# Performance work log

Measured on AMD Instinct MI355X. Metric: run time of the kernel, lower is better.

## Reference

```python
import jax, jax.numpy as jnp
import numpy as np

S, B, D, H = 2048, 2, 1024, 16
DK = D // H  # 64

def setup_inputs() -> dict:
    key0 = jax.random.key(0)
    ks = jax.random.split(key0, 11)
    scale = 0.02
    inp = {
        'query': jax.random.normal(ks[0], (S, B, D), jnp.float32),
        'key':   jax.random.normal(ks[1], (S, B, D), jnp.float32),
        'value': jax.random.normal(ks[2], (S, B, D), jnp.float32),
        # nn.Linear weights stored torch-style [out_features, in_features]
        'Wq': jax.random.normal(ks[3], (H * DK, D), jnp.float32) * scale,
        'bq': jnp.zeros((H * DK,), jnp.float32),
        'Wk': jax.random.normal(ks[4], (H * DK, D), jnp.float32) * scale,
        'bk': jnp.zeros((H * DK,), jnp.float32),
        'Wv': jax.random.normal(ks[5], (H * DK, D), jnp.float32) * scale,
        'bv': jnp.zeros((H * DK,), jnp.float32),
        'Wo': jax.random.normal(ks[6], (D, D), jnp.float32) * scale,
        'bo': jnp.zeros((D,), jnp.float32),
    }
    return inp

def _proj(x, W, b):
    # x: [S,B,D] -> [S,B,H,DK]
    y = jnp.einsum('sbd,ed->sbe', x, W) + b
    return y.reshape(x.shape[0], x.shape[1], H, DK)

def reference(query, key, value, Wq, bq, Wk, bk, Wv, bv, Wo, bo):
    q = _proj(query, Wq, bq)   # [S,B,H,DK]
    k = _proj(key,   Wk, bk)
    v = _proj(value, Wv, bv)
    # NOTE: original forward never applies self.scale -> unscaled QK^T (faithful)
    scores = jnp.einsum('ibhd,jbhd->ijbh', q, k)      # [Sq,Sk,B,H]
    attn = jax.nn.softmax(scores, axis=1)             # softmax over key axis j
    x = jnp.einsum('ijbh,jbhd->ibhd', attn, v)        # [S,B,H,DK]
    x = x.reshape(q.shape[0], q.shape[1], H * DK)     # [S,B,D]
    out = jnp.einsum('sbd,ed->sbe', x, Wo) + bo       # [S,B,D]
    return out
```

## Files before the change

kernel.cpp:

```cpp
#include <hip/hip_runtime.h>
#include <stdint.h>

#define S_LEN  2048
#define BATCH  2
#define DMODEL 1024
#define NHEAD  16
#define DKH    64

typedef __attribute__((ext_vector_type(8))) __bf16 bf16x8;
typedef __attribute__((ext_vector_type(4))) float  f32x4;
typedef unsigned short u16;
typedef unsigned int   u32;

#if __has_builtin(__builtin_amdgcn_exp2f)
#define EXP2(x) __builtin_amdgcn_exp2f(x)
#else
#define EXP2(x) __expf(0.69314718055994531f * (x))
#endif

#define SWAP32(a, b) asm("v_permlane32_swap_b32 %0, %1" : "+v"(a), "+v"(b))
#define SWAP16(a, b) asm("v_permlane16_swap_b32 %0, %1" : "+v"(a), "+v"(b))

__device__ __forceinline__ u16 f2bf(float f) {
  union { float f; u32 u; } v; v.f = f;
  u32 r = v.u + 0x7fffu + ((v.u >> 16) & 1u);
  return (u16)(r >> 16);
}

__global__ void cvt_all(const float4* __restrict__ q, const float4* __restrict__ k,
                        const float4* __restrict__ v,
                        const float4* __restrict__ wq, const float4* __restrict__ wk,
                        const float4* __restrict__ wv, const float4* __restrict__ wo,
                        ushort4* __restrict__ dst) {
  const int NX4 = (S_LEN * BATCH * DMODEL) / 4;
  const int NW4 = (DMODEL * DMODEL) / 4;
  int i = blockIdx.x * blockDim.x + threadIdx.x;
  const float4* src;
  int off;
  if (i < 3 * NX4) {
    src = (i < NX4) ? q : (i < 2 * NX4) ? k : v;
    off = i & (NX4 - 1);
  } else {
    int j = i - 3 * NX4;
    int t = j >> 18;
    src = (t == 0) ? wq : (t == 1) ? wk : (t == 2) ? wv : wo;
    off = j & (NW4 - 1);
  }
  float4 val = src[off];
  ushort4 o;
  o.x = f2bf(val.x); o.y = f2bf(val.y); o.z = f2bf(val.z); o.w = f2bf(val.w);
  dst[i] = o;
}

__global__ __launch_bounds__(256, 2)
void gemm_qkv(const u16* __restrict__ Abase, const u16* __restrict__ Wbase,
              const float* __restrict__ b0, const float* __restrict__ b1,
              const float* __restrict__ b2, u16* __restrict__ Obase) {
  __shared__ __align__(16) u16 As[128 * 32];
  __shared__ __align__(16) u16 Bs[128 * 32];

  const int L = blockIdx.x + (blockIdx.y << 3) + (blockIdx.z << 8);
  const int xcd = L & 7, sl = L >> 3;
  const int z  = sl >> 5;
  const int y  = xcd * 4 + ((sl >> 3) & 3);
  const int nx = sl & 7;

  const u16* A = Abase + (size_t)z * (S_LEN * BATCH * DMODEL);
  const u16* W = Wbase + (size_t)z * (DMODEL * DMODEL);
  const float* bias = (z == 0) ? b0 : (z == 1) ? b1 : b2;
  u16* O = Obase + (size_t)z * (S_LEN * BATCH * DMODEL);
  const float scl = (z == 0) ? 1.4426950408889634f : 1.0f;

  const int tid  = threadIdx.x;
  const int wave = tid >> 6, lane = tid & 63;
  const int quad = lane >> 4, lcol = lane & 15;
  const int m0 = y * 128, n0 = nx * 128;
  const int wm = (wave >> 1) * 64, wn = (wave & 1) * 64;

  f32x4 acc[4][4] = {};

  for (int k0 = 0; k0 < DMODEL; k0 += 32) {
#pragma unroll
    for (int r = 0; r < 2; ++r) {
      int idx = r * 256 + tid;
      int row = idx >> 2, col = (idx & 3) * 8;
      const u16* gA = A + (size_t)(m0 + row) * DMODEL + k0 + col;
      const u16* gW = W + (size_t)(n0 + row) * DMODEL + k0 + col;
      u16* lA = As + (size_t)(r * 256 + (tid & 192)) * 8;
      u16* lB = Bs + (size_t)(r * 256 + (tid & 192)) * 8;
      __builtin_amdgcn_global_load_lds((const __attribute__((address_space(1))) void*)gA,
                                       (__attribute__((address_space(3))) void*)lA, 16, 0, 0);
      __builtin_amdgcn_global_load_lds((const __attribute__((address_space(1))) void*)gW,
                                       (__attribute__((address_space(3))) void*)lB, 16, 0, 0);
    }
    __syncthreads();

    const u16* aBase = As + (wm + lcol) * 32 + quad * 8;
    const u16* bBase = Bs + (wn + lcol) * 32 + quad * 8;
    bf16x8 af[4], bfr[4];
#pragma unroll
    for (int i = 0; i < 4; ++i) af[i]  = *(const bf16x8*)(aBase + i * 16 * 32);
#pragma unroll
    for (int j = 0; j < 4; ++j) bfr[j] = *(const bf16x8*)(bBase + j * 16 * 32);
#pragma unroll
    for (int i = 0; i < 4; ++i)
#pragma unroll
      for (int j = 0; j < 4; ++j)
        acc[i][j] = __builtin_amdgcn_mfma_f32_16x16x32_bf16(af[i], bfr[j], acc[i][j], 0, 0, 0);
    __syncthreads();
  }

#pragma unroll
  for (int i = 0; i < 4; ++i) {
#pragma unroll
    for (int j = 0; j < 4; ++j) {
      int n = n0 + wn + j * 16 + lcol;
      int h = n >> 6, dk = n & 63;
      float bv = bias[n];
#pragma unroll
      for (int r = 0; r < 4; ++r) {
        int m = m0 + wm + i * 16 + quad * 4 + r;
        int s = m >> 1, b = m & 1;
        O[((size_t)(b * NHEAD + h) * S_LEN + s) * DKH + dk] = f2bf((acc[i][j][r] + bv) * scl);
      }
    }
  }
}

__global__ __launch_bounds__(256, 2)
void gemm_o(const u16* __restrict__ A, const u16* __restrict__ W,
            const float* __restrict__ bias, float* __restrict__ O) {
  __shared__ __align__(16) u16 As[128 * 32];
  __shared__ __align__(16) u16 Bs[64 * 32];

  const int L = blockIdx.x + (blockIdx.y << 4);
  const int xcd = L & 7, sl = L >> 3;
  const int y = xcd * 4 + (sl >> 4);
  const int x = sl & 15;

  const int tid  = threadIdx.x;
  const int wave = tid >> 6, lane = tid & 63;
  const int quad = lane >> 4, lcol = lane & 15;
  const int m0 = y * 128, n0 = x * 64;
  const int wm = (wave >> 1) * 64, wn = (wave & 1) * 32;

  f32x4 acc[4][2] = {};

  for (int k0 = 0; k0 < DMODEL; k0 += 32) {
#pragma unroll
    for (int r = 0; r < 2; ++r) {
      int idx = r * 256 + tid;
      int row = idx >> 2, col = (idx & 3) * 8;
      const u16* gA = A + (size_t)(m0 + row) * DMODEL + k0 + col;
      u16* lA = As + (size_t)(r * 256 + (tid & 192)) * 8;
      __builtin_amdgcn_global_load_lds((const __attribute__((address_space(1))) void*)gA,
                                       (__attribute__((address_space(3))) void*)lA, 16, 0, 0);
    }
    {
      int row = tid >> 2, col = (tid & 3) * 8;
      const u16* gW = W + (size_t)(n0 + row) * DMODEL + k0 + col;
      u16* lB = Bs + (size_t)(tid & 192) * 8;
      __builtin_amdgcn_global_load_lds((const __attribute__((address_space(1))) void*)gW,
                                       (__attribute__((address_space(3))) void*)lB, 16, 0, 0);
    }
    __syncthreads();

    const u16* aBase = As + (wm + lcol) * 32 + quad * 8;
    const u16* bBase = Bs + (wn + lcol) * 32 + quad * 8;
    bf16x8 af[4], bfr[2];
#pragma unroll
    for (int i = 0; i < 4; ++i) af[i]  = *(const bf16x8*)(aBase + i * 16 * 32);
#pragma unroll
    for (int j = 0; j < 2; ++j) bfr[j] = *(const bf16x8*)(bBase + j * 16 * 32);
#pragma unroll
    for (int i = 0; i < 4; ++i)
#pragma unroll
      for (int j = 0; j < 2; ++j)
        acc[i][j] = __builtin_amdgcn_mfma_f32_16x16x32_bf16(af[i], bfr[j], acc[i][j], 0, 0, 0);
    __syncthreads();
  }

#pragma unroll
  for (int i = 0; i < 4; ++i) {
#pragma unroll
    for (int j = 0; j < 2; ++j) {
      int n = n0 + wn + j * 16 + lcol;
      float bv = bias[n];
#pragma unroll
      for (int r = 0; r < 4; ++r) {
        int m = m0 + wm + i * 16 + quad * 4 + r;
        O[(size_t)m * DMODEL + n] = acc[i][j][r] + bv;
      }
    }
  }
}

__global__ __launch_bounds__(512, 2)
void attn_kernel(const u16* __restrict__ Q, const u16* __restrict__ K,
                 const u16* __restrict__ V, u16* __restrict__ O) {
  __shared__ __align__(16) u16 smem[9216 + 9216];
  __shared__ float ls2[4][4][16];
  u16* Ks  = smem;
  u16* Vts = smem + 9216;

  const int tid  = threadIdx.x;
  const int wave = tid >> 6, lane = tid & 63;
  const int quad = lane >> 4, lcol = lane & 15;
  const int qg = wave & 3;
  const int kh = wave >> 2;

  const int L = blockIdx.x + (blockIdx.y << 3);
  const int xcd = L & 7, slot = L >> 3;
  const int bh = xcd * 4 + (slot >> 3);
  const int q0 = (slot & 7) * 256;

  const size_t headOff = (size_t)bh * S_LEN * DKH;
  const u16* Qg = Q + headOff;
  const u16* Kg = K + headOff;
  const u16* Vg = V + headOff;

  bf16x8 qf[4][2];
#pragma unroll
  for (int s = 0; s < 4; ++s)
#pragma unroll
    for (int kc = 0; kc < 2; ++kc)
      qf[s][kc] = *(const bf16x8*)(Qg + (size_t)(q0 + qg * 64 + s * 16 + lcol) * DKH +
                                   kc * 32 + quad * 8);

  const int krow  = tid >> 3, kch = tid & 7;
  const int vhalf = lane >> 5, vkp = lane & 31;
  const int vo    = wave;

  uint4 kr0 = *(const uint4*)(Kg + (size_t)krow * DKH + kch * 8);
  uint4 kr1 = *(const uint4*)(Kg + (size_t)(S_LEN / 2 + krow) * DKH + kch * 8);
  uint4 vr0, vr1;
  {
    const u16* vp = Vg + (size_t)(vhalf * (S_LEN / 2) + 2 * vkp) * DKH + 8 * vo;
    vr0 = *(const uint4*)vp;
    vr1 = *(const uint4*)(vp + DKH);
  }

  f32x4 o_acc[4][4] = {};
  float lsum[4] = {0.f, 0.f, 0.f, 0.f};

  for (int it = 0; it < 16; ++it) {
    *(uint4*)(Ks + (size_t)krow * 72 + kch * 8)        = kr0;
    *(uint4*)(Ks + (size_t)(64 + krow) * 72 + kch * 8) = kr1;
    {
      u16* vd = Vts + vhalf * 4608;
#pragma unroll
      for (int jj = 0; jj < 4; ++jj) {
        u32 aw = ((const u32*)&vr0)[jj], bw = ((const u32*)&vr1)[jj];
        *(u32*)(vd + (size_t)(8 * vo + 2 * jj) * 72 + 2 * vkp)     = __builtin_amdgcn_perm(bw, aw, 0x05040100u);
        *(u32*)(vd + (size_t)(8 * vo + 2 * jj + 1) * 72 + 2 * vkp) = __builtin_amdgcn_perm(bw, aw, 0x07060302u);
      }
    }
    __syncthreads();

    if (it < 15) {
      int nb = (it + 1) * 64;
      kr0 = *(const uint4*)(Kg + (size_t)(nb + krow) * DKH + kch * 8);
      kr1 = *(const uint4*)(Kg + (size_t)(S_LEN / 2 + nb + krow) * DKH + kch * 8);
      const u16* vp = Vg + (size_t)(vhalf * (S_LEN / 2) + nb + 2 * vkp) * DKH + 8 * vo;
      vr0 = *(const uint4*)vp;
      vr1 = *(const uint4*)(vp + DKH);
    }

    const u16* kb = Ks  + kh * 64 * 72;
    const u16* vb = Vts + kh * 4608;

#pragma unroll
    for (int g = 0; g < 2; ++g) {
      bf16x8 ak[2][2];
#pragma unroll
      for (int jb = 0; jb < 2; ++jb)
#pragma unroll
        for (int kc = 0; kc < 2; ++kc)
          ak[jb][kc] = *(const bf16x8*)(kb + (g * 32 + jb * 16 + lcol) * 72 + kc * 32 + quad * 8);
      f32x4 sc[2][4] = {};
      __builtin_amdgcn_s_setprio(1);
#pragma unroll
      for (int kc = 0; kc < 2; ++kc)
#pragma unroll
        for (int jb = 0; jb < 2; ++jb)
#pragma unroll
          for (int s = 0; s < 4; ++s)
            sc[jb][s] = __builtin_amdgcn_mfma_f32_16x16x32_bf16(ak[jb][kc], qf[s][kc], sc[jb][s], 0, 0, 0);
      __builtin_amdgcn_s_setprio(0);

      bf16x8 pa[4];
#pragma unroll
      for (int s = 0; s < 4; ++s) {
        u32 ww[2][2];
#pragma unroll
        for (int jb = 0; jb < 2; ++jb) {
          float p0 = EXP2(sc[jb][s][0]);
          float p1 = EXP2(sc[jb][s][1]);
          float p2 = EXP2(sc[jb][s][2]);
          float p3 = EXP2(sc[jb][s][3]);
          lsum[s] += (p0 + p1) + (p2 + p3);
          asm("v_cvt_pk_bf16_f32 %0, %1, %2" : "=v"(ww[jb][0]) : "v"(p0), "v"(p1));
          asm("v_cvt_pk_bf16_f32 %0, %1, %2" : "=v"(ww[jb][1]) : "v"(p2), "v"(p3));
        }
        u32 a0 = ww[0][0], b0 = ww[1][0];
        SWAP32(a0, b0); SWAP16(a0, b0);
        u32 a1 = ww[0][1], b1 = ww[1][1];
        SWAP32(a1, b1); SWAP16(a1, b1);
        union { u32 u[4]; bf16x8 v; } f;
        f.u[0] = a0; f.u[1] = a1; f.u[2] = b0; f.u[3] = b1;
        pa[s] = f.v;
      }

      bf16x8 bv[4];
#pragma unroll
      for (int jd = 0; jd < 4; ++jd)
        bv[jd] = *(const bf16x8*)(vb + (jd * 16 + lcol) * 72 + g * 32 + quad * 8);
      __builtin_amdgcn_s_setprio(1);
#pragma unroll
      for (int s = 0; s < 4; ++s)
#pragma unroll
        for (int jd = 0; jd < 4; ++jd)
          o_acc[s][jd] = __builtin_amdgcn_mfma_f32_16x16x32_bf16(pa[s], bv[jd], o_acc[s][jd], 0, 0, 0);
      __builtin_amdgcn_s_setprio(0);
    }

    __syncthreads();
  }

#pragma unroll
  for (int s = 0; s < 4; ++s) {
    lsum[s] += __shfl_xor(lsum[s], 16);
    lsum[s] += __shfl_xor(lsum[s], 32);
  }

  float* scr = (float*)smem;
  const int cbase = (qg * 64 + lane) * 32;
  if (kh == 1) {
#pragma unroll
    for (int s = 0; s < 2; ++s)
#pragma unroll
      for (int jd = 0; jd < 4; ++jd)
        *(f32x4*)(scr + cbase + (s * 4 + jd) * 4) = o_acc[s][jd];
    if (lane < 16) {
#pragma unroll
      for (int s = 0; s < 4; ++s) ls2[qg][s][lane] = lsum[s];
    }
  }
  __syncthreads();
  if (kh == 0) {
#pragma unroll
    for (int s = 0; s < 2; ++s)
#pragma unroll
      for (int jd = 0; jd < 4; ++jd)
        o_acc[s][jd] += *(const f32x4*)(scr + cbase + (s * 4 + jd) * 4);
  }
  __syncthreads();
  if (kh == 1) {
#pragma unroll
    for (int s = 2; s < 4; ++s)
#pragma unroll
      for (int jd = 0; jd < 4; ++jd)
        *(f32x4*)(scr + cbase + ((s - 2) * 4 + jd) * 4) = o_acc[s][jd];
  }
  __syncthreads();
  if (kh == 0) {
#pragma unroll
    for (int s = 2; s < 4; ++s)
#pragma unroll
      for (int jd = 0; jd < 4; ++jd)
        o_acc[s][jd] += *(const f32x4*)(scr + cbase + ((s - 2) * 4 + jd) * 4);

    float tot[4];
#pragma unroll
    for (int s = 0; s < 4; ++s) tot[s] = lsum[s] + ls2[qg][s][lcol];

    const int b = bh >> 4, hh = bh & 15;
#pragma unroll
    for (int s = 0; s < 4; ++s) {
#pragma unroll
      for (int r = 0; r < 4; ++r) {
        float inv = 1.f / __shfl(tot[s], quad * 4 + r);
        int sq = q0 + qg * 64 + s * 16 + quad * 4 + r;
#pragma unroll
        for (int jd = 0; jd < 4; ++jd) {
          int dk = jd * 16 + lcol;
          O[((size_t)(sq * BATCH + b)) * DMODEL + hh * DKH + dk] = f2bf(o_acc[s][jd][r] * inv);
        }
      }
    }
  }
}

extern "C" void kernel_launch(void* const* d_in, const int* in_sizes, int n_in,
                              void* d_out, int out_size, void* d_ws, size_t ws_size,
                              hipStream_t stream) {
  const float* q  = (const float*)d_in[0];
  const float* k  = (const float*)d_in[1];
  const float* v  = (const float*)d_in[2];
  const float* Wq = (const float*)d_in[3];
  const float* bq = (const float*)d_in[4];
  const float* Wk = (const float*)d_in[5];
  const float* bk = (const float*)d_in[6];
  const float* Wv = (const float*)d_in[7];
  const float* bv = (const float*)d_in[8];
  const float* Wo = (const float*)d_in[9];
  const float* bo = (const float*)d_in[10];

  const int NX = S_LEN * BATCH * DMODEL;
  const int NW = DMODEL * DMODEL;

  u16* ws  = (u16*)d_ws;
  u16* Xq  = ws;
  u16* Wqb = Xq  + 3 * (size_t)NX;
  u16* Qb  = Wqb + 4 * (size_t)NW;
  u16* Xo  = Qb  + 3 * (size_t)NX;

  u16* Wob = Wqb + 3 * (size_t)NW;
  u16* Kb  = Qb + NX, *Vb = Qb + 2 * (size_t)NX;

  const int n4 = (3 * NX + 4 * NW) / 4;
  cvt_all<<<n4 / 256, 256, 0, stream>>>((const float4*)q, (const float4*)k, (const float4*)v,
                                        (const float4*)Wq, (const float4*)Wk, (const float4*)Wv,
                                        (const float4*)Wo, (ushort4*)ws);

  dim3 gqkv(DMODEL / 128, (S_LEN * BATCH) / 128, 3);
  gemm_qkv<<<gqkv, 256, 0, stream>>>(Xq, Wqb, bq, bk, bv, Qb);

  dim3 ga(S_LEN / 256, BATCH * NHEAD);
  attn_kernel<<<ga, 512, 0, stream>>>(Qb, Kb, Vb, Xo);

  dim3 go(DMODEL / 64, (S_LEN * BATCH) / 128);
  gemm_o<<<go, 256, 0, stream>>>(Xo, Wob, bo, (float*)d_out);
}
```

Before: 214.3 us.

## Double-buffer attention K/V in LDS with direct global-to-LDS K loads

Each attention block now covers 128 queries instead of 256, so the grid doubles and launch bounds target more resident blocks. K tiles are loaded straight into LDS with global_load_lds using an XOR swizzle instead of padding, and K and V use double-buffered LDS so one barrier per iteration suffices. The V transpose write is moved after compute to overlap with it, and the final reduction drops to a single exchange round. This adds more K/V reloads per head and LDS pressure, and relies on the swizzle and buffer indexing being correct.

```diff
diff --git a/kernel.cpp b/kernel.cpp
--- a/kernel.cpp
+++ b/kernel.cpp
@@ -195,13 +195,12 @@
   }
 }
 
-__global__ __launch_bounds__(512, 2)
+__global__ __launch_bounds__(512, 4)
 void attn_kernel(const u16* __restrict__ Q, const u16* __restrict__ K,
                  const u16* __restrict__ V, u16* __restrict__ O) {
-  __shared__ __align__(16) u16 smem[9216 + 9216];
-  __shared__ float ls2[4][4][16];
-  u16* Ks  = smem;
-  u16* Vts = smem + 9216;
+  __shared__ __align__(16) u16 Ks[2][128 * 64];
+  __shared__ __align__(16) u16 Vts[2][2 * 4608];
+  __shared__ float ls2[4][2][16];
 
   const int tid  = threadIdx.x;
   const int wave = tid >> 6, lane = tid & 63;
@@ -209,65 +208,72 @@
   const int qg = wave & 3;
   const int kh = wave >> 2;
 
-  const int L = blockIdx.x + (blockIdx.y << 3);
+  const int L = blockIdx.x + (blockIdx.y << 4);
   const int xcd = L & 7, slot = L >> 3;
-  const int bh = xcd * 4 + (slot >> 3);
-  const int q0 = (slot & 7) * 256;
+  const int bh = xcd * 4 + (slot >> 4);
+  const int q0 = (slot & 15) * 128;
 
   const size_t headOff = (size_t)bh * S_LEN * DKH;
   const u16* Qg = Q + headOff;
   const u16* Kg = K + headOff;
   const u16* Vg = V + headOff;
 
-  bf16x8 qf[4][2];
-#pragma unroll
-  for (int s = 0; s < 4; ++s)
+  bf16x8 qf[2][2];
+#pragma unroll
+  for (int s = 0; s < 2; ++s)
 #pragma unroll
     for (int kc = 0; kc < 2; ++kc)
-      qf[s][kc] = *(const bf16x8*)(Qg + (size_t)(q0 + qg * 64 + s * 16 + lcol) * DKH +
+      qf[s][kc] = *(const bf16x8*)(Qg + (size_t)(q0 + qg * 32 + s * 16 + lcol) * DKH +
                                    kc * 32 + quad * 8);
 
-  const int krow  = tid >> 3, kch = tid & 7;
-  const int vhalf = lane >> 5, vkp = lane & 31;
-  const int vo    = wave;
-
-  uint4 kr0 = *(const uint4*)(Kg + (size_t)krow * DKH + kch * 8);
-  uint4 kr1 = *(const uint4*)(Kg + (size_t)(S_LEN / 2 + krow) * DKH + kch * 8);
-  uint4 vr0, vr1;
+  const int krow = tid >> 3;
+  const int kcs  = (((tid & 7) ^ ((tid >> 3) & 7))) * 8;
+  const int kdst = (tid & 448) * 8;
+  const int vhalf = lane >> 5, vkp = lane & 31, vo = wave;
+
   {
     const u16* vp = Vg + (size_t)(vhalf * (S_LEN / 2) + 2 * vkp) * DKH + 8 * vo;
-    vr0 = *(const uint4*)vp;
-    vr1 = *(const uint4*)(vp + DKH);
-  }
-
-  f32x4 o_acc[4][4] = {};
-  float lsum[4] = {0.f, 0.f, 0.f, 0.f};
+    uint4 vr0 = *(const uint4*)vp;
+    uint4 vr1 = *(const uint4*)(vp + DKH);
+    __builtin_amdgcn_global_load_lds(
+        (const __attribute__((address_space(1))) void*)(Kg + (size_t)krow * DKH + kcs),
+        (__attribute__((address_space(3))) void*)(Ks[0] + kdst), 16, 0, 0);
+    __builtin_amdgcn_global_load_lds(
+        (const __attribute__((address_space(1))) void*)(Kg + (size_t)(S_LEN / 2 + krow) * DKH + kcs),
+        (__attribute__((address_space(3))) void*)(Ks[0] + 4096 + kdst), 16, 0, 0);
+    u16* vd = Vts[0] + vhalf * 4608;
+#pragma unroll
+    for (int jj = 0; jj < 4; ++jj) {
+      u32 aw = ((const u32*)&vr0)[jj], bw = ((const u32*)&vr1)[jj];
+      *(u32*)(vd + (size_t)(8 * vo + 2 * jj) * 72 + 2 * vkp)     = __builtin_amdgcn_perm(bw, aw, 0x05040100u);
+      *(u32*)(vd + (size_t)(8 * vo + 2 * jj + 1) * 72 + 2 * vkp) = __builtin_amdgcn_perm(bw, aw, 0x07060302u);
+    }
+  }
+
+  f32x4 o_acc[2][4] = {};
+  float lsum[2] = {0.f, 0.f};
 
   for (int it = 0; it < 16; ++it) {
-    *(uint4*)(Ks + (size_t)krow * 72 + kch * 8)        = kr0;
-    *(uint4*)(Ks + (size_t)(64 + krow) * 72 + kch * 8) = kr1;
-    {
-      u16* vd = Vts + vhalf * 4608;
-#pragma unroll
-      for (int jj = 0; jj < 4; ++jj) {
-        u32 aw = ((const u32*)&vr0)[jj], bw = ((const u32*)&vr1)[jj];
-        *(u32*)(vd + (size_t)(8 * vo + 2 * jj) * 72 + 2 * vkp)     = __builtin_amdgcn_perm(bw, aw, 0x05040100u);
-        *(u32*)(vd + (size_t)(8 * vo + 2 * jj + 1) * 72 + 2 * vkp) = __builtin_amdgcn_perm(bw, aw, 0x07060302u);
-      }
-    }
+    const int cur = it & 1;
     __syncthreads();
 
-    if (it < 15) {
-      int nb = (it + 1) * 64;
-      kr0 = *(const uint4*)(Kg + (size_t)(nb + krow) * DKH + kch * 8);
-      kr1 = *(const uint4*)(Kg + (size_t)(S_LEN / 2 + nb + krow) * DKH + kch * 8);
+    uint4 vr0, vr1;
+    const bool has = (it < 15);
+    if (has) {
+      const int nb = (it + 1) * 64;
       const u16* vp = Vg + (size_t)(vhalf * (S_LEN / 2) + nb + 2 * vkp) * DKH + 8 * vo;
       vr0 = *(const uint4*)vp;
       vr1 = *(const uint4*)(vp + DKH);
-    }
-
-    const u16* kb = Ks  + kh * 64 * 72;
-    const u16* vb = Vts + kh * 4608;
+      __builtin_amdgcn_global_load_lds(
+          (const __attribute__((address_space(1))) void*)(Kg + (size_t)(nb + krow) * DKH + kcs),
+          (__attribute__((address_space(3))) void*)(Ks[cur ^ 1] + kdst), 16, 0, 0);
+      __builtin_amdgcn_global_load_lds(
+          (const __attribute__((address_space(1))) void*)(Kg + (size_t)(S_LEN / 2 + nb + krow) * DKH + kcs),
+          (__attribute__((address_space(3))) void*)(Ks[cur ^ 1] + 4096 + kdst), 16, 0, 0);
+    }
+
+    const u16* kb = Ks[cur] + kh * 4096;
+    const u16* vb = Vts[cur] + kh * 4608;
 
 #pragma unroll
     for (int g = 0; g < 2; ++g) {
@@ -276,21 +282,22 @@
       for (int jb = 0; jb < 2; ++jb)
 #pragma unroll
         for (int kc = 0; kc < 2; ++kc)
-          ak[jb][kc] = *(const bf16x8*)(kb + (g * 32 + jb * 16 + lcol) * 72 + kc * 32 + quad * 8);
-      f32x4 sc[2][4] = {};
+          ak[jb][kc] = *(const bf16x8*)(kb + (g * 32 + jb * 16 + lcol) * 64 +
+                                        ((((kc << 2) | quad) ^ (lcol & 7)) << 3));
+      f32x4 sc[2][2] = {};
       __builtin_amdgcn_s_setprio(1);
 #pragma unroll
       for (int kc = 0; kc < 2; ++kc)
 #pragma unroll
         for (int jb = 0; jb < 2; ++jb)
 #pragma unroll
-          for (int s = 0; s < 4; ++s)
+          for (int s = 0; s < 2; ++s)
             sc[jb][s] = __builtin_amdgcn_mfma_f32_16x16x32_bf16(ak[jb][kc], qf[s][kc], sc[jb][s], 0, 0, 0);
       __builtin_amdgcn_s_setprio(0);
 
-      bf16x8 pa[4];
-#pragma unroll
-      for (int s = 0; s < 4; ++s) {
+      bf16x8 pa[2];
+#pragma unroll
+      for (int s = 0; s < 2; ++s) {
         u32 ww[2][2];
 #pragma unroll
         for (int jb = 0; jb < 2; ++jb) {
@@ -317,24 +324,34 @@
         bv[jd] = *(const bf16x8*)(vb + (jd * 16 + lcol) * 72 + g * 32 + quad * 8);
       __builtin_amdgcn_s_setprio(1);
 #pragma unroll
-      for (int s = 0; s < 4; ++s)
+      for (int s = 0; s < 2; ++s)
 #pragma unroll
         for (int jd = 0; jd < 4; ++jd)
           o_acc[s][jd] = __builtin_amdgcn_mfma_f32_16x16x32_bf16(pa[s], bv[jd], o_acc[s][jd], 0, 0, 0);
       __builtin_amdgcn_s_setprio(0);
     }
 
-    __syncthreads();
-  }
-
-#pragma unroll
-  for (int s = 0; s < 4; ++s) {
+    if (has) {
+      u16* vd = Vts[cur ^ 1] + vhalf * 4608;
+#pragma unroll
+      for (int jj = 0; jj < 4; ++jj) {
+        u32 aw = ((const u32*)&vr0)[jj], bw = ((const u32*)&vr1)[jj];
+        *(u32*)(vd + (size_t)(8 * vo + 2 * jj) * 72 + 2 * vkp)     = __builtin_amdgcn_perm(bw, aw, 0x05040100u);
+        *(u32*)(vd + (size_t)(8 * vo + 2 * jj + 1) * 72 + 2 * vkp) = __builtin_amdgcn_perm(bw, aw, 0x07060302u);
+      }
+    }
+  }
+
+  __syncthreads();
+
+#pragma unroll
+  for (int s = 0; s < 2; ++s) {
     lsum[s] += __shfl_xor(lsum[s], 16);
     lsum[s] += __shfl_xor(lsum[s], 32);
   }
 
-  float* scr = (float*)smem;
-  const int cbase = (qg * 64 + lane) * 32;
+  float* scr = (float*)Vts;
+  const int cbase = (qg * 64 + lane) * 36;
   if (kh == 1) {
 #pragma unroll
     for (int s = 0; s < 2; ++s)
@@ -343,7 +360,7 @@
         *(f32x4*)(scr + cbase + (s * 4 + jd) * 4) = o_acc[s][jd];
     if (lane < 16) {
 #pragma unroll
-      for (int s = 0; s < 4; ++s) ls2[qg][s][lane] = lsum[s];
+      for (int s = 0; s < 2; ++s) ls2[qg][s][lane] = lsum[s];
     }
   }
   __syncthreads();
@@ -353,34 +370,18 @@
 #pragma unroll
       for (int jd = 0; jd < 4; ++jd)
         o_acc[s][jd] += *(const f32x4*)(scr + cbase + (s * 4 + jd) * 4);
-  }
-  __syncthreads();
-  if (kh == 1) {
-#pragma unroll
-    for (int s = 2; s < 4; ++s)
-#pragma unroll
-      for (int jd = 0; jd < 4; ++jd)
-        *(f32x4*)(scr + cbase + ((s - 2) * 4 + jd) * 4) = o_acc[s][jd];
-  }
-  __syncthreads();
-  if (kh == 0) {
-#pragma unroll
-    for (int s = 2; s < 4; ++s)
-#pragma unroll
-      for (int jd = 0; jd < 4; ++jd)
-        o_acc[s][jd] += *(const f32x4*)(scr + cbase + ((s - 2) * 4 + jd) * 4);
-
-    float tot[4];
-#pragma unroll
-    for (int s = 0; s < 4; ++s) tot[s] = lsum[s] + ls2[qg][s][lcol];
+
+    float tot[2];
+#pragma unroll
+    for (int s = 0; s < 2; ++s) tot[s] = lsum[s] + ls2[qg][s][lcol];
 
     const int b = bh >> 4, hh = bh & 15;
 #pragma unroll
-    for (int s = 0; s < 4; ++s) {
+    for (int s = 0; s < 2; ++s) {
 #pragma unroll
       for (int r = 0; r < 4; ++r) {
         float inv = 1.f / __shfl(tot[s], quad * 4 + r);
-        int sq = q0 + qg * 64 + s * 16 + quad * 4 + r;
+        int sq = q0 + qg * 32 + s * 16 + quad * 4 + r;
 #pragma unroll
         for (int jd = 0; jd < 4; ++jd) {
           int dk = jd * 16 + lcol;
@@ -426,7 +427,7 @@
   dim3 gqkv(DMODEL / 128, (S_LEN * BATCH) / 128, 3);
   gemm_qkv<<<gqkv, 256, 0, stream>>>(Xq, Wqb, bq, bk, bv, Qb);
 
-  dim3 ga(S_LEN / 256, BATCH * NHEAD);
+  dim3 ga(S_LEN / 128, BATCH * NHEAD);
   attn_kernel<<<ga, 512, 0, stream>>>(Qb, Kb, Vb, Xo);
 
   dim3 go(DMODEL / 64, (S_LEN * BATCH) / 128);
```

Result: no change. 216.2 us (+0.9%).
